# Kernel optimization log

Measured on AMD Instinct MI355X. Metric: run time of the kernel, lower is better.

Reference implementation:

```python
import jax, jax.numpy as jnp
import numpy as np

B, S, HID = 1, 2048, 2048
H, NOPE, ROPE, VDIM = 16, 128, 64, 128
QR, KVR = 1536, 512
IH, ID = 16, 128
TOPK = 512
THETA = 10000.0
EPS = 1e-6
SCALE = (NOPE + ROPE) ** -0.5
NEG = -1e9


def _cos_sin(s, dim, dtype):
    inv = 1.0 / (THETA ** (np.arange(0, dim, 2, dtype=np.float32) / dim))
    t = np.arange(s, dtype=np.float32)
    f = np.outer(t, inv)
    emb = np.concatenate([f, f], -1)
    return jnp.asarray(np.cos(emb), dtype), jnp.asarray(np.sin(emb), dtype)


def _rope(x, cos, sin):
    # x: [b,s,h,d]; cos/sin: [s,d]; NeoX-style rotate_half
    x1, x2 = jnp.split(x, 2, axis=-1)
    rot = jnp.concatenate([-x2, x1], axis=-1)
    return x * cos[None, :, None, :] + rot * sin[None, :, None, :]


def _rmsnorm(x, w):
    v = jnp.mean(x.astype(jnp.float32) ** 2, -1, keepdims=True)
    return (x.astype(jnp.float32) * jax.lax.rsqrt(v + EPS)).astype(x.dtype) * w


def _layernorm(x, w, b):
    m = jnp.mean(x, -1, keepdims=True)
    v = jnp.var(x, -1, keepdims=True)
    return (x - m) * jax.lax.rsqrt(v + EPS) * w + b


def setup_inputs() -> dict:
    key = jax.random.key(0)
    ks = jax.random.split(key, 12)
    g = lambda k, shp: jax.random.normal(k, shp, jnp.float32) * 0.02
    return {
        'hidden_states': jax.random.normal(ks[0], (B, S, HID), jnp.float32),
        'q_a_w': g(ks[1], (QR, HID)),
        'q_a_ln_w': jnp.ones((QR,), jnp.float32),
        'q_b_w': g(ks[2], (H * (NOPE + ROPE), QR)),
        'kv_a_w': g(ks[3], (KVR + ROPE, HID)),
        'kv_a_ln_w': jnp.ones((KVR,), jnp.float32),
        'kv_b_w': g(ks[4], (H * (NOPE + VDIM), KVR)),
        'o_w': g(ks[5], (HID, H * VDIM)),
        'idx_wq_b_w': g(ks[6], (IH * ID, QR)),
        'idx_wk_w': g(ks[7], (ID, HID)),
        'idx_kn_w': jnp.ones((ID,), jnp.float32),
        'idx_kn_b': jnp.zeros((ID,), jnp.float32),
        'idx_wproj_w': g(ks[8], (IH, HID)),
    }


def reference(hidden_states, q_a_w, q_a_ln_w, q_b_w, kv_a_w, kv_a_ln_w, kv_b_w, o_w,
              idx_wq_b_w, idx_wk_w, idx_kn_w, idx_kn_b, idx_wproj_w):
    b, s, _ = hidden_states.shape
    cos, sin = _cos_sin(s, ROPE, hidden_states.dtype)

    # --- MLA projections ---
    qr = _rmsnorm(hidden_states @ q_a_w.T, q_a_ln_w)                 # [b,s,QR]
    q = (qr @ q_b_w.T).reshape(b, s, H, NOPE + ROPE)
    q_nope, q_pe = q[..., :NOPE], q[..., NOPE:]
    q_pe = _rope(q_pe, cos, sin)
    ckv = hidden_states @ kv_a_w.T                                   # [b,s,KVR+ROPE]
    c_kv, k_pe = ckv[..., :KVR], ckv[..., KVR:]
    k_pe = _rope(k_pe[:, :, None, :], cos, sin)                      # [b,s,1,ROPE]
    kv = (_rmsnorm(c_kv, kv_a_ln_w) @ kv_b_w.T).reshape(b, s, H, NOPE + VDIM)
    k_nope, v = kv[..., :NOPE], kv[..., NOPE:]

    # --- DSA indexer: per-token importance scores ---
    iq = (qr @ idx_wq_b_w.T).reshape(b, s, IH, ID)
    iq = jnp.concatenate([_rope(iq[..., :ROPE], cos, sin), iq[..., ROPE:]], -1)
    ik = _layernorm(hidden_states @ idx_wk_w.T, idx_kn_w, idx_kn_b)  # [b,s,ID]
    ik_pe = _rope(ik[:, :, None, :ROPE], cos, sin)[:, :, 0, :]
    ik = jnp.concatenate([ik_pe, ik[..., ROPE:]], -1)
    iw = (hidden_states @ idx_wproj_w.T) * (IH ** -0.5)              # [b,s,IH]
    idx_scores = jnp.einsum('bqh,bhqk->bqk', iw,
                            jax.nn.relu(jnp.einsum('bqhd,bkd->bhqk', iq, ik)))
    causal = jnp.tril(jnp.ones((s, s), bool))
    idx_scores = jnp.where(causal[None], idx_scores, -jnp.inf)
    _, top_idx = jax.lax.top_k(idx_scores, TOPK)                     # [b,s,TOPK]
    bi = jnp.arange(b)[:, None, None]
    qi = jnp.arange(s)[None, :, None]
    keep = jnp.zeros((b, s, s), bool).at[bi, qi, top_idx].set(True)
    allowed = keep & causal[None]                                    # [b,s,s]

    # --- sparse top-k attention (top-k mask to -inf before softmax) ---
    qh = jnp.concatenate([q_nope, q_pe], -1)                         # [b,s,H,192]
    kh = jnp.concatenate([k_nope, jnp.broadcast_to(k_pe, (b, s, H, ROPE))], -1)
    scores = jnp.einsum('bqhd,bkhd->bhqk', qh, kh) * SCALE
    scores = jnp.where(allowed[:, None], scores, NEG)
    attn = jax.nn.softmax(scores, -1)
    out = jnp.einsum('bhqk,bkhd->bqhd', attn, v).reshape(b, s, H * VDIM)
    return out @ o_w.T
```

## Files before the change

### kernel.cpp

```cpp
#include <hip/hip_runtime.h>
#include <hip/hip_bf16.h>
#include <math.h>

#define SEQ 2048
#define HIDD 2048
#define QRANK 1536
#define KVRANK 512
#define TOPK 512
#define EPSF 1e-6f
#define SCALE_ATTN 0.07216878364870323f
#define NCAT 1680

typedef __attribute__((ext_vector_type(8))) short short8v;
typedef __attribute__((ext_vector_type(4))) short short4v;
typedef __attribute__((ext_vector_type(4))) float f32x4;

__device__ inline unsigned short f2bf(float f) {
    unsigned u = __float_as_uint(f);
    unsigned r = (u + 0x7FFFu + ((u >> 16) & 1u)) >> 16;
    return (unsigned short)r;
}
__device__ inline float bf2f(unsigned short b) {
    return __uint_as_float(((unsigned)b) << 16);
}
__device__ inline void split2(float x, unsigned short& h, unsigned short& l) {
    h = f2bf(x);
    l = f2bf(x - bf2f(h));
}

__device__ inline short4v ds_read_tr16(const void* p) {
#if __has_builtin(__builtin_amdgcn_ds_read_tr16_b64)
    return __builtin_amdgcn_ds_read_tr16_b64((short4v*)p);
#else
    const unsigned short* u = (const unsigned short*)p;
    short4v r;
    r[0] = (short)u[0]; r[1] = (short)u[16]; r[2] = (short)u[32]; r[3] = (short)u[48];
    return r;
#endif
}

__global__ void rope_table_kernel(float* __restrict__ cos_t, float* __restrict__ sin_t) {
    int s = blockIdx.x;
    int i = threadIdx.x;
    double inv = pow(10000.0, -((double)(2 * i)) / 64.0);
    double f = (double)s * inv;
    cos_t[s * 32 + i] = (float)cos(f);
    sin_t[s * 32 + i] = (float)sin(f);
}

__global__ __launch_bounds__(256) void cvt_bf16_4_kernel(
    const float* __restrict__ a, int na4, const float* __restrict__ b, int nb4,
    const float* __restrict__ c, int nc4, const float* __restrict__ d, int nd4,
    unsigned short* __restrict__ oa, unsigned short* __restrict__ ob,
    unsigned short* __restrict__ oc, unsigned short* __restrict__ od)
{
    int total = na4 + nb4 + nc4 + nd4;
    for (int i = blockIdx.x * 256 + threadIdx.x; i < total; i += gridDim.x * 256) {
        const float* src; unsigned short* dst; int j = i;
        if (j < na4) { src = a; dst = oa; }
        else if ((j -= na4) < nb4) { src = b; dst = ob; }
        else if ((j -= nb4) < nc4) { src = c; dst = oc; }
        else { j -= nc4; src = d; dst = od; }
        float4 v = ((const float4*)src)[j];
        ushort4 o;
        o.x = f2bf(v.x); o.y = f2bf(v.y); o.z = f2bf(v.z); o.w = f2bf(v.w);
        ((ushort4*)dst)[j] = o;
    }
}

__global__ __launch_bounds__(256) void wkt_kernel(const float* __restrict__ kvb,
                                                  unsigned short* __restrict__ wkt) {
    __shared__ float t[128][129];
    int h = blockIdx.x, n0 = blockIdx.y * 128;
    int tid = threadIdx.x;
    for (int it = tid; it < 128 * 32; it += 256) {
        int d = it >> 5, c4 = it & 31;
        float4 v = *(const float4*)(kvb + ((size_t)(h * 256 + d)) * 512 + n0 + c4 * 4);
        t[d][c4 * 4 + 0] = v.x; t[d][c4 * 4 + 1] = v.y;
        t[d][c4 * 4 + 2] = v.z; t[d][c4 * 4 + 3] = v.w;
    }
    __syncthreads();
    for (int it = tid; it < 128 * 32; it += 256) {
        int n = it >> 5, dc = it & 31;
        ushort4 o;
        o.x = f2bf(t[dc * 4 + 0][n]); o.y = f2bf(t[dc * 4 + 1][n]);
        o.z = f2bf(t[dc * 4 + 2][n]); o.w = f2bf(t[dc * 4 + 3][n]);
        *(ushort4*)(wkt + ((size_t)h * 512 + n0 + n) * 128 + dc * 4) = o;
    }
}

__global__ __launch_bounds__(256) void gemm_cat_split_kernel(
    const float* __restrict__ hidden, const float* __restrict__ q_a_w,
    const float* __restrict__ idx_wk_w, const float* __restrict__ idx_wproj_w,
    float* __restrict__ ccat)
{
    __shared__ __align__(16) unsigned short Ah[128 * 32], Al[128 * 32];
    __shared__ __align__(16) unsigned short Bh[128 * 32], Bl[128 * 32];
    int tid = threadIdx.x;
    int l = tid & 63, w = tid >> 6;
    int wr = w >> 1, wc = w & 1;
    int m0 = blockIdx.x * 128, n0 = blockIdx.y * 128;
    f32x4 acc[4][4] = {};
    for (int k0 = 0; k0 < HIDD; k0 += 32) {
        __syncthreads();
#pragma unroll
        for (int i = 0; i < 2; ++i) {
            int idx = tid + i * 256;
            int r = idx >> 2, cc = idx & 3;
            int sw = cc ^ (r & 3);
            {
                const float* src = hidden + (size_t)(m0 + r) * HIDD + k0 + cc * 8;
                float4 f0 = *(const float4*)src, f1 = *(const float4*)(src + 4);
                float xs[8] = {f0.x, f0.y, f0.z, f0.w, f1.x, f1.y, f1.z, f1.w};
                short8v dh, dl;
#pragma unroll
                for (int e = 0; e < 8; ++e) {
                    unsigned short hh, ll; split2(xs[e], hh, ll);
                    dh[e] = (short)hh; dl[e] = (short)ll;
                }
                *(short8v*)&Ah[r * 32 + sw * 8] = dh;
                *(short8v*)&Al[r * 32 + sw * 8] = dl;
            }
            {
                int gb = n0 + r; if (gb > NCAT - 1) gb = NCAT - 1;
                float scale = 1.f;
                const float* src;
                if (gb < 1536) src = q_a_w + (size_t)gb * HIDD;
                else if (gb < 1664) src = idx_wk_w + (size_t)(gb - 1536) * HIDD;
                else { src = idx_wproj_w + (size_t)(gb - 1664) * HIDD; scale = 0.25f; }
                src += k0 + cc * 8;
                float4 f0 = *(const float4*)src, f1 = *(const float4*)(src + 4);
                float xs[8] = {f0.x, f0.y, f0.z, f0.w, f1.x, f1.y, f1.z, f1.w};
                short8v dh, dl;
#pragma unroll
                for (int e = 0; e < 8; ++e) {
                    unsigned short hh, ll; split2(xs[e] * scale, hh, ll);
                    dh[e] = (short)hh; dl[e] = (short)ll;
                }
                *(short8v*)&Bh[r * 32 + sw * 8] = dh;
                *(short8v*)&Bl[r * 32 + sw * 8] = dl;
            }
        }
        __syncthreads();
        short8v avh[4], avl[4];
#pragma unroll
        for (int mt = 0; mt < 4; ++mt) {
            int row = wr * 64 + mt * 16 + (l & 15);
            int ch = (l >> 4) ^ (row & 3);
            avh[mt] = *(const short8v*)&Ah[row * 32 + ch * 8];
            avl[mt] = *(const short8v*)&Al[row * 32 + ch * 8];
        }
#pragma unroll
        for (int nt = 0; nt < 4; ++nt) {
            int row = wc * 64 + nt * 16 + (l & 15);
            int ch = (l >> 4) ^ (row & 3);
            short8v bvh = *(const short8v*)&Bh[row * 32 + ch * 8];
            short8v bvl = *(const short8v*)&Bl[row * 32 + ch * 8];
#pragma unroll
            for (int mt = 0; mt < 4; ++mt) {
                acc[mt][nt] = __builtin_amdgcn_mfma_f32_16x16x32_bf16(avh[mt], bvh, acc[mt][nt], 0, 0, 0);
                acc[mt][nt] = __builtin_amdgcn_mfma_f32_16x16x32_bf16(avh[mt], bvl, acc[mt][nt], 0, 0, 0);
                acc[mt][nt] = __builtin_amdgcn_mfma_f32_16x16x32_bf16(avl[mt], bvh, acc[mt][nt], 0, 0, 0);
            }
        }
    }
#pragma unroll
    for (int mt = 0; mt < 4; ++mt)
#pragma unroll
        for (int nt = 0; nt < 4; ++nt)
#pragma unroll
            for (int i = 0; i < 4; ++i) {
                int gm = m0 + wr * 64 + mt * 16 + (l >> 4) * 4 + i;
                int gn = n0 + wc * 64 + nt * 16 + (l & 15);
                if (gn < NCAT) ccat[(size_t)gm * NCAT + gn] = acc[mt][nt][i];
            }
}

__global__ __launch_bounds__(256) void gemm_iq_split_kernel(
    const float* __restrict__ qr, const float* __restrict__ wq,
    const float* __restrict__ cos_t, const float* __restrict__ sin_t,
    unsigned short* __restrict__ iqh, unsigned short* __restrict__ iql)
{
    __shared__ __align__(16) unsigned short Ah[128 * 32], Al[128 * 32];
    __shared__ __align__(16) unsigned short Bh[128 * 32], Bl[128 * 32];
    int tid = threadIdx.x;
    int l = tid & 63, w = tid >> 6;
    int wr = w >> 1, wc = w & 1;
    int m0 = blockIdx.x * 128, n0 = blockIdx.y * 128;
    int hh_ = blockIdx.y;
    f32x4 acc[4][4] = {};
    for (int k0 = 0; k0 < QRANK; k0 += 32) {
        __syncthreads();
#pragma unroll
        for (int i = 0; i < 2; ++i) {
            int idx = tid + i * 256;
            int r = idx >> 2, cc = idx & 3;
            int sw = cc ^ (r & 3);
            {
                const float* src = qr + (size_t)(m0 + r) * QRANK + k0 + cc * 8;
                float4 f0 = *(const float4*)src, f1 = *(const float4*)(src + 4);
                float xs[8] = {f0.x, f0.y, f0.z, f0.w, f1.x, f1.y, f1.z, f1.w};
                short8v dh, dl;
#pragma unroll
                for (int e = 0; e < 8; ++e) {
                    unsigned short h2, l2; split2(xs[e], h2, l2);
                    dh[e] = (short)h2; dl[e] = (short)l2;
                }
                *(short8v*)&Ah[r * 32 + sw * 8] = dh;
                *(short8v*)&Al[r * 32 + sw * 8] = dl;
            }
            {
                const float* src = wq + (size_t)(n0 + r) * QRANK + k0 + cc * 8;
                float4 f0 = *(const float4*)src, f1 = *(const float4*)(src + 4);
                float xs[8] = {f0.x, f0.y, f0.z, f0.w, f1.x, f1.y, f1.z, f1.w};
                short8v dh, dl;
#pragma unroll
                for (int e = 0; e < 8; ++e) {
                    unsigned short h2, l2; split2(xs[e], h2, l2);
                    dh[e] = (short)h2; dl[e] = (short)l2;
                }
                *(short8v*)&Bh[r * 32 + sw * 8] = dh;
                *(short8v*)&Bl[r * 32 + sw * 8] = dl;
            }
        }
        __syncthreads();
        short8v avh[4], avl[4];
#pragma unroll
        for (int mt = 0; mt < 4; ++mt) {
            int row = wr * 64 + mt * 16 + (l & 15);
            int ch = (l >> 4) ^ (row & 3);
            avh[mt] = *(const short8v*)&Ah[row * 32 + ch * 8];
            avl[mt] = *(const short8v*)&Al[row * 32 + ch * 8];
        }
#pragma unroll
        for (int nt = 0; nt < 4; ++nt) {
            int row = wc * 64 + nt * 16 + (l & 15);
            int ch = (l >> 4) ^ (row & 3);
            short8v bvh = *(const short8v*)&Bh[row * 32 + ch * 8];
            short8v bvl = *(const short8v*)&Bl[row * 32 + ch * 8];
#pragma unroll
            for (int mt = 0; mt < 4; ++mt) {
                acc[mt][nt] = __builtin_amdgcn_mfma_f32_16x16x32_bf16(avh[mt], bvh, acc[mt][nt], 0, 0, 0);
                acc[mt][nt] = __builtin_amdgcn_mfma_f32_16x16x32_bf16(avh[mt], bvl, acc[mt][nt], 0, 0, 0);
                acc[mt][nt] = __builtin_amdgcn_mfma_f32_16x16x32_bf16(avl[mt], bvh, acc[mt][nt], 0, 0, 0);
            }
        }
    }
    if (wc == 0) {
#pragma unroll
        for (int mt = 0; mt < 4; ++mt)
#pragma unroll
            for (int nt = 0; nt < 2; ++nt)
#pragma unroll
                for (int i = 0; i < 4; ++i) {
                    int q = m0 + wr * 64 + mt * 16 + (l >> 4) * 4 + i;
                    int dd = nt * 16 + (l & 15);
                    float c = cos_t[q * 32 + dd], s = sin_t[q * 32 + dd];
                    float x1 = acc[mt][nt][i], x2 = acc[mt][nt + 2][i];
                    acc[mt][nt][i] = x1 * c - x2 * s;
                    acc[mt][nt + 2][i] = x2 * c + x1 * s;
                }
    }
#pragma unroll
    for (int mt = 0; mt < 4; ++mt)
#pragma unroll
        for (int nt = 0; nt < 4; ++nt)
#pragma unroll
            for (int i = 0; i < 4; ++i) {
                int q = m0 + wr * 64 + mt * 16 + (l >> 4) * 4 + i;
                int d = wc * 64 + nt * 16 + (l & 15);
                size_t idx = ((size_t)q * 16 + hh_) * 128 + d;
                unsigned short h2, l2; split2(acc[mt][nt][i], h2, l2);
                iqh[idx] = h2; iql[idx] = l2;
            }
}

template <typename TA, typename TC>
__global__ __launch_bounds__(256) void mfma_nt_kernel(
    const TA* __restrict__ A, const unsigned short* __restrict__ B, TC* __restrict__ C,
    int M, int N, int K, int lda, int ldb, int ldc, long ab, long bb, long cb,
    const float* __restrict__ cos_t, const float* __restrict__ sin_t, int rope_mode)
{
    __shared__ __align__(16) unsigned short Asl[128 * 32];
    __shared__ __align__(16) unsigned short Bsl[128 * 32];
    int z = blockIdx.z;
    const TA* Az = A + (size_t)z * ab;
    const unsigned short* Bz = B + (size_t)z * bb;
    TC* Cz = C + (size_t)z * cb;
    int tid = threadIdx.x;
    int l = tid & 63, w = tid >> 6;
    int wr = w >> 1, wc = w & 1;
    int m0 = blockIdx.x * 128, n0 = blockIdx.y * 128;
    f32x4 acc[4][4] = {};

    for (int k0 = 0; k0 < K; k0 += 32) {
        __syncthreads();
#pragma unroll
        for (int i = 0; i < 2; ++i) {
            int idx = tid + i * 256;
            int r = idx >> 2, cc = idx & 3;
            int sw = cc ^ (r & 3);
            {
                short8v d;
                const TA* src = Az + (size_t)(m0 + r) * lda + k0 + cc * 8;
                if constexpr (sizeof(TA) == 2) {
                    d = *(const short8v*)src;
                } else {
                    float4 f0 = *(const float4*)src;
                    float4 f1 = *(const float4*)(src + 4);
                    d[0] = (short)f2bf(f0.x); d[1] = (short)f2bf(f0.y);
                    d[2] = (short)f2bf(f0.z); d[3] = (short)f2bf(f0.w);
                    d[4] = (short)f2bf(f1.x); d[5] = (short)f2bf(f1.y);
                    d[6] = (short)f2bf(f1.z); d[7] = (short)f2bf(f1.w);
                }
                *(short8v*)&Asl[r * 32 + sw * 8] = d;
            }
            {
                int gb = n0 + r; if (gb > N - 1) gb = N - 1;
                short8v d = *(const short8v*)(Bz + (size_t)gb * ldb + k0 + cc * 8);
                *(short8v*)&Bsl[r * 32 + sw * 8] = d;
            }
        }
        __syncthreads();
        short8v av[4], bv[4];
#pragma unroll
        for (int mt = 0; mt < 4; ++mt) {
            int row = wr * 64 + mt * 16 + (l & 15);
            int ch = (l >> 4) ^ (row & 3);
            av[mt] = *(const short8v*)&Asl[row * 32 + ch * 8];
        }
#pragma unroll
        for (int nt = 0; nt < 4; ++nt) {
            int row = wc * 64 + nt * 16 + (l & 15);
            int ch = (l >> 4) ^ (row & 3);
            bv[nt] = *(const short8v*)&Bsl[row * 32 + ch * 8];
        }
#pragma unroll
        for (int mt = 0; mt < 4; ++mt)
#pragma unroll
            for (int nt = 0; nt < 4; ++nt)
                acc[mt][nt] = __builtin_amdgcn_mfma_f32_16x16x32_bf16(av[mt], bv[nt], acc[mt][nt], 0, 0, 0);
    }
    if (rope_mode) {
        int gcol64 = (n0 >> 6) + wc;
        bool dorope = (rope_mode == 1) ? ((gcol64 % 3) == 2) : (gcol64 == 8);
        if (dorope) {
#pragma unroll
            for (int mt = 0; mt < 4; ++mt)
#pragma unroll
                for (int nt = 0; nt < 2; ++nt)
#pragma unroll
                    for (int i = 0; i < 4; ++i) {
                        int q = m0 + wr * 64 + mt * 16 + (l >> 4) * 4 + i;
                        int dd = nt * 16 + (l & 15);
                        float c = cos_t[q * 32 + dd], sn = sin_t[q * 32 + dd];
                        float x1 = acc[mt][nt][i], x2 = acc[mt][nt + 2][i];
                        acc[mt][nt][i] = x1 * c - x2 * sn;
                        acc[mt][nt + 2][i] = x2 * c + x1 * sn;
                    }
        }
    }
#pragma unroll
    for (int mt = 0; mt < 4; ++mt) {
#pragma unroll
        for (int nt = 0; nt < 4; ++nt) {
#pragma unroll
            for (int i = 0; i < 4; ++i) {
                int gm = m0 + wr * 64 + mt * 16 + (l >> 4) * 4 + i;
                int gn = n0 + wc * 64 + nt * 16 + (l & 15);
                if (gn < N) {
                    float v = acc[mt][nt][i];
                    if constexpr (sizeof(TC) == 4) Cz[(size_t)gm * ldc + gn] = v;
                    else Cz[(size_t)gm * ldc + gn] = f2bf(v);
                }
            }
        }
    }
}

__global__ __launch_bounds__(256) void rmsnorm_kernel(
    const float* __restrict__ in, const float* __restrict__ w, float* __restrict__ out,
    unsigned short* __restrict__ bf_out, int n, int in_stride)
{
    int row = blockIdx.x, tid = threadIdx.x;
    const float* x = in + (size_t)row * in_stride;
    float4 v[2];
    int cnt = 0;
    float ss = 0.f;
    int nf4 = n >> 2;
    for (int i = tid; i < nf4; i += 256) {
        float4 t = *(const float4*)(x + i * 4);
        v[cnt++] = t;
        ss += t.x * t.x + t.y * t.y + t.z * t.z + t.w * t.w;
    }
#pragma unroll
    for (int m = 32; m; m >>= 1) ss += __shfl_xor(ss, m);
    __shared__ float red[8];
    int wid = tid >> 6;
    if ((tid & 63) == 0) red[wid] = ss;
    __syncthreads();
    if (tid == 0) {
        float s = red[0] + red[1] + red[2] + red[3];
        red[4] = rsqrtf(s / (float)n + EPSF);
    }
    __syncthreads();
    float scale = red[4];
    cnt = 0;
    for (int i = tid; i < nf4; i += 256) {
        float4 t = v[cnt++];
        float4 wv = *(const float4*)(w + i * 4);
        float4 o;
        o.x = t.x * scale * wv.x; o.y = t.y * scale * wv.y;
        o.z = t.z * scale * wv.z; o.w = t.w * scale * wv.w;
        *(float4*)(out + (size_t)row * n + i * 4) = o;
        if (bf_out) {
            ushort4 ob;
            ob.x = f2bf(o.x); ob.y = f2bf(o.y); ob.z = f2bf(o.z); ob.w = f2bf(o.w);
            *(ushort4*)(bf_out + (size_t)row * n + i * 4) = ob;
        }
    }
}

__global__ __launch_bounds__(256) void rmsnorm_khg_kernel(
    const float* __restrict__ ckv, const float* __restrict__ w,
    unsigned short* __restrict__ khg)
{
    int row = blockIdx.x, tid = threadIdx.x;
    const float* x = ckv + (size_t)row * 576;
    float4 v = make_float4(0.f, 0.f, 0.f, 0.f);
    float ss = 0.f;
    if (tid < 128) {
        v = *(const float4*)(x + tid * 4);
        ss = v.x * v.x + v.y * v.y + v.z * v.z + v.w * v.w;
    }
#pragma unroll
    for (int mm = 32; mm; mm >>= 1) ss += __shfl_xor(ss, mm);
    __shared__ float red[8];
    if ((tid & 63) == 0) red[tid >> 6] = ss;
    __syncthreads();
    if (tid == 0) red[4] = rsqrtf((red[0] + red[1] + red[2] + red[3]) * (1.f / 512.f) + EPSF);
    __syncthreads();
    float scale = red[4];
    if (tid < 128) {
        float4 wv = *(const float4*)(w + tid * 4);
        ushort4 ob;
        ob.x = f2bf(v.x * scale * wv.x); ob.y = f2bf(v.y * scale * wv.y);
        ob.z = f2bf(v.z * scale * wv.z); ob.w = f2bf(v.w * scale * wv.w);
        *(ushort4*)(khg + (size_t)row * 576 + tid * 4) = ob;
    } else if (tid < 192) {
        khg[(size_t)row * 576 + 512 + (tid - 128)] = f2bf(x[512 + tid - 128]);
    }
}

__global__ __launch_bounds__(64) void ln_rope_split_kernel(
    const float* __restrict__ in, int stride,
    const float* __restrict__ w, const float* __restrict__ b,
    const float* __restrict__ cos_t, const float* __restrict__ sin_t,
    unsigned short* __restrict__ ikh, unsigned short* __restrict__ ikl)
{
    int row = blockIdx.x, tid = threadIdx.x;
    const float* x = in + (size_t)row * stride;
    float x0 = x[tid], x1 = x[tid + 64];
    float s = x0 + x1, ss = x0 * x0 + x1 * x1;
#pragma unroll
    for (int m = 32; m; m >>= 1) { s += __shfl_xor(s, m); ss += __shfl_xor(ss, m); }
    float mean = s * (1.f / 128.f);
    float var = ss * (1.f / 128.f) - mean * mean;
    float r = rsqrtf(var + EPSF);
    float n0 = (x0 - mean) * r * w[tid] + b[tid];
    float n1 = (x1 - mean) * r * w[tid + 64] + b[tid + 64];
    float c = cos_t[row * 32 + (tid & 31)], sn = sin_t[row * 32 + (tid & 31)];
    float other = __shfl_xor(n0, 32);
    float r0 = (tid < 32) ? (n0 * c - other * sn) : (n0 * c + other * sn);
    unsigned short h2, l2;
    split2(r0, h2, l2);
    ikh[(size_t)row * 128 + tid] = h2; ikl[(size_t)row * 128 + tid] = l2;
    split2(n1, h2, l2);
    ikh[(size_t)row * 128 + 64 + tid] = h2; ikl[(size_t)row * 128 + 64 + tid] = l2;
}

__global__ __launch_bounds__(256) void idx_scores_mfma_kernel(
    const unsigned short* __restrict__ iqh, const unsigned short* __restrict__ iql,
    const unsigned short* __restrict__ ikh, const unsigned short* __restrict__ ikl,
    const float* __restrict__ iwsrc, int iw_stride,
    float* __restrict__ scores)
{
    int q0 = blockIdx.x * 64, k0 = blockIdx.y * 64;
    int tid = threadIdx.x;
    if (k0 > q0 + 63) {
        for (int t = tid; t < 64 * 64; t += 256) {
            int r = t >> 6, c = t & 63;
            scores[(size_t)(q0 + r) * SEQ + k0 + c] = -INFINITY;
        }
        return;
    }
    __shared__ __align__(16) unsigned short skh[64 * 128], skl[64 * 128];
    __shared__ __align__(16) unsigned short sqh[64 * 128], sql[64 * 128];
    __shared__ float iws[64][16];
    int l = tid & 63, w = tid >> 6;
    for (int it = tid; it < 64 * 16; it += 256) {
        int r = it >> 4, c = it & 15;
        int sw = c ^ (r & 15);
        *(short8v*)&skh[r * 128 + sw * 8] = *(const short8v*)(ikh + (size_t)(k0 + r) * 128 + c * 8);
        *(short8v*)&skl[r * 128 + sw * 8] = *(const short8v*)(ikl + (size_t)(k0 + r) * 128 + c * 8);
    }
    {
        int r = tid >> 2, c = tid & 3;
        *(float4*)&iws[r][c * 4] = *(const float4*)(iwsrc + (size_t)(q0 + r) * iw_stride + c * 4);
    }
    __syncthreads();
    short8v bhr[4][4], blr[4][4];
#pragma unroll
    for (int nt = 0; nt < 4; ++nt)
#pragma unroll
        for (int ks = 0; ks < 4; ++ks) {
            int brow = nt * 16 + (l & 15);
            int bch = ((l >> 4) + ks * 4) ^ (brow & 15);
            bhr[nt][ks] = *(const short8v*)&skh[brow * 128 + bch * 8];
            blr[nt][ks] = *(const short8v*)&skl[brow * 128 + bch * 8];
        }
    f32x4 acc[4] = {};
    for (int h = 0; h < 16; ++h) {
        __syncthreads();
        for (int it = tid; it < 64 * 16; it += 256) {
            int r = it >> 4, c = it & 15;
            int sw = c ^ (r & 15);
            size_t base = ((size_t)(q0 + r) * 16 + h) * 128 + c * 8;
            *(short8v*)&sqh[r * 128 + sw * 8] = *(const short8v*)(iqh + base);
            *(short8v*)&sql[r * 128 + sw * 8] = *(const short8v*)(iql + base);
        }
        __syncthreads();
        f32x4 dot[4] = {};
#pragma unroll
        for (int ks = 0; ks < 4; ++ks) {
            int arow = w * 16 + (l & 15);
            int ach = ((l >> 4) + ks * 4) ^ (arow & 15);
            short8v ah = *(const short8v*)&sqh[arow * 128 + ach * 8];
            short8v al = *(const short8v*)&sql[arow * 128 + ach * 8];
#pragma unroll
            for (int nt = 0; nt < 4; ++nt) {
                dot[nt] = __builtin_amdgcn_mfma_f32_16x16x32_bf16(ah, bhr[nt][ks], dot[nt], 0, 0, 0);
                dot[nt] = __builtin_amdgcn_mfma_f32_16x16x32_bf16(ah, blr[nt][ks], dot[nt], 0, 0, 0);
                dot[nt] = __builtin_amdgcn_mfma_f32_16x16x32_bf16(al, bhr[nt][ks], dot[nt], 0, 0, 0);
            }
        }
#pragma unroll
        for (int nt = 0; nt < 4; ++nt)
#pragma unroll
            for (int i = 0; i < 4; ++i) {
                float wv = iws[w * 16 + (l >> 4) * 4 + i][h];
                acc[nt][i] += wv * fmaxf(dot[nt][i], 0.f);
            }
    }
#pragma unroll
    for (int nt = 0; nt < 4; ++nt)
#pragma unroll
        for (int i = 0; i < 4; ++i) {
            int q = q0 + w * 16 + (l >> 4) * 4 + i;
            int k = k0 + nt * 16 + (l & 15);
            scores[(size_t)q * SEQ + k] = (k <= q) ? acc[nt][i] : -INFINITY;
        }
}

__global__ __launch_bounds__(1024) void topk_kernel(
    const float* __restrict__ scores, int* __restrict__ sel)
{
    int qi = blockIdx.x, tid = threadIdx.x;
    __shared__ unsigned long long keys[2048];
    const float* srow = scores + (size_t)qi * SEQ;
#pragma unroll
    for (int r = 0; r < 2; ++r) {
        int k = tid + r * 1024;
        unsigned u = __float_as_uint(srow[k]);
        unsigned mv = (u & 0x80000000u) ? ~u : (u | 0x80000000u);
        keys[k] = ((unsigned long long)mv << 32) | (unsigned)(2047 - k);
    }
    for (int ksz = 2; ksz <= 2048; ksz <<= 1) {
        for (int j = ksz >> 1; j > 0; j >>= 1) {
            __syncthreads();
#pragma unroll 1
            for (int r = 0; r < 2; ++r) {
                int i = tid + r * 1024;
                int ixj = i ^ j;
                if (ixj > i) {
                    unsigned long long a = keys[i], b = keys[ixj];
                    bool dir = ((i & ksz) == 0);
                    if ((a < b) == dir) { keys[i] = b; keys[ixj] = a; }
                }
            }
        }
    }
    __syncthreads();
    if (tid < TOPK) {
        int k = 2047 - (int)(keys[tid] & 0xFFFFFFFFu);
        sel[(size_t)qi * TOPK + tid] = (tid <= qi) ? k : -1;
    }
}

__global__ __launch_bounds__(256) void attn_mfma_kernel(
    const unsigned short* __restrict__ qabs,
    const float* __restrict__ qsrc,
    const unsigned short* __restrict__ khg,
    const int* __restrict__ sel,
    unsigned short* __restrict__ ocomp)
{
    __shared__ __align__(16) char smem[77568];
    unsigned short* plds = (unsigned short*)(smem + 74752);
    float* smax = (float*)(smem + 76800);
    float* ssum = (float*)(smem + 77056);
    int* selb   = (int*)(smem + 77312);

    const int qi = blockIdx.x;
    const int tid = threadIdx.x;
    const int l = tid & 63, w = tid >> 6;
    const int lg = l >> 4, lr = l & 15;
    const int nv = min(TOPK, qi + 1);
    const int ntile = (nv + 63) >> 6;
    const int krow = w * 16 + lr;

    short8v aq[18];
    {
        const unsigned short* qa = qabs + ((size_t)qi * 16 + lr) * 512 + lg * 8;
#pragma unroll
        for (int ks = 0; ks < 16; ++ks)
            aq[ks] = *(const short8v*)(qa + ks * 32);
        const float* qp = qsrc + (size_t)qi * 3072 + lr * 192 + 128 + lg * 8;
#pragma unroll
        for (int ks = 0; ks < 2; ++ks) {
            float4 f0 = *(const float4*)(qp + ks * 32);
            float4 f1 = *(const float4*)(qp + ks * 32 + 4);
            short8v d;
            d[0] = (short)f2bf(f0.x); d[1] = (short)f2bf(f0.y);
            d[2] = (short)f2bf(f0.z); d[3] = (short)f2bf(f0.w);
            d[4] = (short)f2bf(f1.x); d[5] = (short)f2bf(f1.y);
            d[6] = (short)f2bf(f1.z); d[7] = (short)f2bf(f1.w);
            aq[16 + ks] = d;
        }
    }

    const int sbase = krow * 32 + (lg >> 1) * 2080 + (lg & 1) * 16;
    const int vboff = w * 16640 + lg * 256 + lr * 2;

    float m[4] = {-1e30f, -1e30f, -1e30f, -1e30f};
    float lsum[4] = {0.f, 0.f, 0.f, 0.f};
    f32x4 oacc[8] = {};

    for (int t = 0; t < ntile; ++t) {
        const int j0 = t * 64;
        __syncthreads();
        if (tid < 64) {
            int sv = sel[(size_t)qi * TOPK + j0 + tid];
            selb[tid] = sv < 0 ? 0 : sv;
        }
        __syncthreads();
        for (int it = tid; it < 64 * 64; it += 256) {
            int key = it >> 6, c = it & 63;
            short8v v = *(const short8v*)(khg + (size_t)selb[key] * 576 + c * 8);
            *(short8v*)(smem + (c >> 1) * 2080 + key * 32 + (c & 1) * 16) = v;
        }
        for (int it = tid; it < 64 * 8; it += 256) {
            int key = it >> 3, c = it & 7;
            short8v v = *(const short8v*)(khg + (size_t)selb[key] * 576 + 512 + c * 8);
            *(short8v*)(smem + 66560 + ((key * 128 + c * 16) ^ ((key & 7) << 4))) = v;
        }
        __syncthreads();
        f32x4 s = {};
#pragma unroll
        for (int ks = 0; ks < 16; ++ks) {
            short8v b = *(const short8v*)(smem + sbase + ks * 4160);
            s = __builtin_amdgcn_mfma_f32_16x16x32_bf16(aq[ks], b, s, 0, 0, 0);
        }
#pragma unroll
        for (int ks = 0; ks < 2; ++ks) {
            short8v b = *(const short8v*)(smem + 66560 +
                ((krow * 128 + ks * 64 + lg * 16) ^ ((krow & 7) << 4)));
            s = __builtin_amdgcn_mfma_f32_16x16x32_bf16(aq[16 + ks], b, s, 0, 0, 0);
        }
        bool kvalid = (j0 + krow) < nv;
#pragma unroll
        for (int i = 0; i < 4; ++i)
            s[i] = kvalid ? s[i] * SCALE_ATTN : -1e30f;
        float tm[4];
#pragma unroll
        for (int i = 0; i < 4; ++i) tm[i] = s[i];
#pragma unroll
        for (int sh = 1; sh < 16; sh <<= 1)
#pragma unroll
            for (int i = 0; i < 4; ++i) tm[i] = fmaxf(tm[i], __shfl_xor(tm[i], sh));
        if (lr == 0) *(float4*)&smax[w * 16 + lg * 4] = make_float4(tm[0], tm[1], tm[2], tm[3]);
        __syncthreads();
        float mn[4], scl[4];
#pragma unroll
        for (int i = 0; i < 4; ++i) {
            int h = lg * 4 + i;
            float tmax = fmaxf(fmaxf(smax[h], smax[16 + h]), fmaxf(smax[32 + h], smax[48 + h]));
            mn[i] = fmaxf(m[i], tmax);
            scl[i] = __expf(m[i] - mn[i]);
            m[i] = mn[i];
        }
        float p[4], rs[4];
#pragma unroll
        for (int i = 0; i < 4; ++i) { p[i] = __expf(s[i] - mn[i]); rs[i] = p[i]; }
#pragma unroll
        for (int sh = 1; sh < 16; sh <<= 1)
#pragma unroll
            for (int i = 0; i < 4; ++i) rs[i] += __shfl_xor(rs[i], sh);
        if (lr == 0) *(float4*)&ssum[w * 16 + lg * 4] = make_float4(rs[0], rs[1], rs[2], rs[3]);
        {
            ushort4 pb;
            pb.x = f2bf(p[0]); pb.y = f2bf(p[1]); pb.z = f2bf(p[2]); pb.w = f2bf(p[3]);
            *(ushort4*)&plds[(w * 16 + lr) * 16 + lg * 4] = pb;
        }
        __syncthreads();
#pragma unroll
        for (int i = 0; i < 4; ++i) {
            int h = lg * 4 + i;
            float ts = ssum[h] + ssum[16 + h] + ssum[32 + h] + ssum[48 + h];
            lsum[i] = lsum[i] * scl[i] + ts;
        }
#pragma unroll
        for (int nt = 0; nt < 8; ++nt)
#pragma unroll
            for (int i = 0; i < 4; ++i) oacc[nt][i] *= scl[i];
#pragma unroll
        for (int kb = 0; kb < 2; ++kb) {
            short8v af;
#pragma unroll
            for (int j = 0; j < 8; ++j)
                af[j] = (short)plds[(kb * 32 + lg * 8 + j) * 16 + lr];
#pragma unroll
            for (int nt = 0; nt < 8; ++nt) {
                const char* a = smem + vboff + kb * 1024 + nt * 2080;
                short4v t0 = ds_read_tr16(a);
                short4v t1 = ds_read_tr16(a + 128);
                short8v bf = __builtin_shufflevector(t0, t1, 0, 1, 2, 3, 4, 5, 6, 7);
                oacc[nt] = __builtin_amdgcn_mfma_f32_16x16x32_bf16(af, bf, oacc[nt], 0, 0, 0);
            }
        }
    }
    float inv[4];
#pragma unroll
    for (int i = 0; i < 4; ++i) inv[i] = 1.f / lsum[i];
    unsigned short* ob = ocomp + (size_t)qi * 16 * 512;
#pragma unroll
    for (int nt = 0; nt < 8; ++nt) {
        int d = w * 128 + nt * 16 + lr;
#pragma unroll
        for (int i = 0; i < 4; ++i) {
            int h = lg * 4 + i;
            ob[h * 512 + d] = f2bf(oacc[nt][i] * inv[i]);
        }
    }
}

extern "C" void kernel_launch(void* const* d_in, const int* in_sizes, int n_in,
                              void* d_out, int out_size, void* d_ws, size_t ws_size,
                              hipStream_t stream) {
    (void)in_sizes; (void)n_in; (void)out_size; (void)ws_size;
    const float* hidden      = (const float*)d_in[0];
    const float* q_a_w       = (const float*)d_in[1];
    const float* q_a_ln_w    = (const float*)d_in[2];
    const float* q_b_w       = (const float*)d_in[3];
    const float* kv_a_w      = (const float*)d_in[4];
    const float* kv_a_ln_w   = (const float*)d_in[5];
    const float* kv_b_w      = (const float*)d_in[6];
    const float* o_w         = (const float*)d_in[7];
    const float* idx_wq_b_w  = (const float*)d_in[8];
    const float* idx_wk_w    = (const float*)d_in[9];
    const float* idx_kn_w    = (const float*)d_in[10];
    const float* idx_kn_b    = (const float*)d_in[11];
    const float* idx_wproj_w = (const float*)d_in[12];
    float* out = (float*)d_out;

    char* ws = (char*)d_ws;
    size_t off = 0;
    auto alloc = [&](size_t nbytes) -> void* {
        void* p = ws + off;
        off = (off + nbytes + 255) & ~(size_t)255;
        return p;
    };
    float* cos_t = (float*)alloc((size_t)SEQ * 32 * 4);
    float* sin_t = (float*)alloc((size_t)SEQ * 32 * 4);
    float* qbuf  = (float*)alloc((size_t)SEQ * 3072 * 4);
    float* ckv   = (float*)alloc((size_t)SEQ * 576 * 4);
    int*   sel   = (int*)alloc((size_t)SEQ * TOPK * 4);
    unsigned short* khg      = (unsigned short*)alloc((size_t)SEQ * 576 * 2);
    unsigned short* attno_bf = (unsigned short*)alloc((size_t)SEQ * 2048 * 2);
    unsigned short* qr_bf    = (unsigned short*)alloc((size_t)SEQ * QRANK * 2);
    unsigned short* q_b_bf   = (unsigned short*)alloc((size_t)3072 * QRANK * 2);
    unsigned short* kv_a_bf  = (unsigned short*)alloc((size_t)576 * HIDD * 2);
    unsigned short* o_w_bf   = (unsigned short*)alloc((size_t)HIDD * 2048 * 2);
    unsigned short* kv_b_bf  = (unsigned short*)alloc((size_t)4096 * 512 * 2);
    unsigned short* wkt      = (unsigned short*)alloc((size_t)16 * 512 * 128 * 2);
    size_t mark = off;
    float* qr    = (float*)alloc((size_t)SEQ * QRANK * 4);
    float* ccat  = (float*)alloc((size_t)SEQ * NCAT * 4);
    float* scores = (float*)alloc((size_t)SEQ * SEQ * 4);
    unsigned short* iqh = (unsigned short*)alloc((size_t)SEQ * 2048 * 2);
    unsigned short* iql = (unsigned short*)alloc((size_t)SEQ * 2048 * 2);
    unsigned short* ikh = (unsigned short*)alloc((size_t)SEQ * 128 * 2);
    unsigned short* ikl = (unsigned short*)alloc((size_t)SEQ * 128 * 2);
    off = mark;
    unsigned short* qabsb = (unsigned short*)alloc((size_t)SEQ * 16 * 512 * 2);
    unsigned short* ocomp = (unsigned short*)alloc((size_t)SEQ * 16 * 512 * 2);

    rope_table_kernel<<<dim3(SEQ), dim3(32), 0, stream>>>(cos_t, sin_t);

    cvt_bf16_4_kernel<<<2048, 256, 0, stream>>>(
        q_b_w, 3072 * QRANK / 4, kv_a_w, 576 * HIDD / 4,
        o_w, HIDD * 2048 / 4, kv_b_w, 4096 * 512 / 4,
        q_b_bf, kv_a_bf, o_w_bf, kv_b_bf);
    wkt_kernel<<<dim3(16, 4), 256, 0, stream>>>(kv_b_w, wkt);

    gemm_cat_split_kernel<<<dim3(16, 14), 256, 0, stream>>>(hidden, q_a_w, idx_wk_w, idx_wproj_w, ccat);

    rmsnorm_kernel<<<SEQ, 256, 0, stream>>>(ccat, q_a_ln_w, qr, qr_bf, QRANK, NCAT);

    ln_rope_split_kernel<<<SEQ, 64, 0, stream>>>(ccat + 1536, NCAT, idx_kn_w, idx_kn_b, cos_t, sin_t, ikh, ikl);

    mfma_nt_kernel<unsigned short, float><<<dim3(16, 24, 1), 256, 0, stream>>>(
        qr_bf, q_b_bf, qbuf, SEQ, 3072, QRANK, QRANK, QRANK, 3072, 0L, 0L, 0L,
        cos_t, sin_t, 1);

    mfma_nt_kernel<float, float><<<dim3(16, 5, 1), 256, 0, stream>>>(
        hidden, kv_a_bf, ckv, SEQ, 576, HIDD, HIDD, HIDD, 576, 0L, 0L, 0L,
        cos_t, sin_t, 2);
    rmsnorm_khg_kernel<<<SEQ, 256, 0, stream>>>(ckv, kv_a_ln_w, khg);

    gemm_iq_split_kernel<<<dim3(16, 16), 256, 0, stream>>>(qr, idx_wq_b_w, cos_t, sin_t, iqh, iql);

    idx_scores_mfma_kernel<<<dim3(32, 32), 256, 0, stream>>>(iqh, iql, ikh, ikl, ccat + 1664, NCAT, scores);
    topk_kernel<<<SEQ, 1024, 0, stream>>>(scores, sel);

    mfma_nt_kernel<float, unsigned short><<<dim3(16, 4, 16), 256, 0, stream>>>(
        qbuf, wkt, qabsb, SEQ, 512, 128, 3072, 128, 16 * 512,
        192L, 512L * 128L, 512L, nullptr, nullptr, 0);

    attn_mfma_kernel<<<SEQ, 256, 0, stream>>>(qabsb, qbuf, khg, sel, ocomp);

    mfma_nt_kernel<unsigned short, unsigned short><<<dim3(16, 1, 16), 256, 0, stream>>>(
        ocomp, kv_b_bf + (size_t)128 * 512, attno_bf, SEQ, 128, 512,
        16 * 512, 512, 2048, 512L, 256L * 512L, 128L, nullptr, nullptr, 0);

    mfma_nt_kernel<unsigned short, float><<<dim3(16, 16, 1), 256, 0, stream>>>(
        attno_bf, o_w_bf, out, SEQ, HIDD, 2048, 2048, 2048, HIDD, 0L, 0L, 0L,
        nullptr, nullptr, 0);
}
```

Measured before the change: 882.8 us.

## Pre-split fp32 operands to bf16 hi/lo and prefetch attention gathers into registers

Adds a conversion kernel that splits hidden states and the concatenated projection weights into bf16 high/low halves once, instead of inside every GEMM tile load. It also has rmsnorm emit the low half of qr so the indexer GEMM can load bf16 pairs directly. Separately, the sparse attention kernel now prefetches the next tile's gathered K/V rows into registers while the current tile computes, which removes one barrier and the shared-memory index buffer. The cost is extra workspace, an added pass over the weights each call, and higher register pressure in the attention kernel.

```diff
diff --git a/kernel.cpp b/kernel.cpp
--- a/kernel.cpp
+++ b/kernel.cpp
@@ -68,6 +68,48 @@
     }
 }
 
+__global__ __launch_bounds__(256) void cvt_split3_kernel(
+    const float* __restrict__ hidden, const float* __restrict__ q_a_w,
+    const float* __restrict__ idx_wk_w, const float* __restrict__ idx_wproj_w,
+    const float* __restrict__ wq,
+    unsigned short* __restrict__ hidh, unsigned short* __restrict__ hidl,
+    unsigned short* __restrict__ catwh, unsigned short* __restrict__ catwl,
+    unsigned short* __restrict__ wqh, unsigned short* __restrict__ wql)
+{
+    const int nhid4 = HIDD * HIDD / 4;
+    const int ncat4 = NCAT * HIDD / 4;
+    const int nwq4  = HIDD * QRANK / 4;
+    int total = nhid4 + ncat4 + nwq4;
+    for (int i = blockIdx.x * 256 + threadIdx.x; i < total; i += gridDim.x * 256) {
+        int j = i;
+        const float4* s4;
+        unsigned short *dh, *dl;
+        float scale = 1.f;
+        if (j < nhid4) {
+            s4 = (const float4*)hidden + j; dh = hidh; dl = hidl;
+        } else if ((j -= nhid4) < ncat4) {
+            int row = (j * 4) >> 11;
+            dh = catwh; dl = catwl;
+            if (row < 1536) s4 = (const float4*)q_a_w + j;
+            else if (row < 1664) s4 = (const float4*)idx_wk_w + (j - 1536 * 512);
+            else { s4 = (const float4*)idx_wproj_w + (j - 1664 * 512); scale = 0.25f; }
+        } else {
+            j -= ncat4;
+            s4 = (const float4*)wq + j; dh = wqh; dl = wql;
+        }
+        float4 v = *s4;
+        float xs[4] = {v.x * scale, v.y * scale, v.z * scale, v.w * scale};
+        ushort4 oh, ol;
+        unsigned short h2, l2;
+        split2(xs[0], h2, l2); oh.x = h2; ol.x = l2;
+        split2(xs[1], h2, l2); oh.y = h2; ol.y = l2;
+        split2(xs[2], h2, l2); oh.z = h2; ol.z = l2;
+        split2(xs[3], h2, l2); oh.w = h2; ol.w = l2;
+        ((ushort4*)dh)[j] = oh;
+        ((ushort4*)dl)[j] = ol;
+    }
+}
+
 __global__ __launch_bounds__(256) void wkt_kernel(const float* __restrict__ kvb,
                                                   unsigned short* __restrict__ wkt) {
     __shared__ float t[128][129];
@@ -92,6 +134,8 @@
 __global__ __launch_bounds__(256) void gemm_cat_split_kernel(
     const float* __restrict__ hidden, const float* __restrict__ q_a_w,
     const float* __restrict__ idx_wk_w, const float* __restrict__ idx_wproj_w,
+    const unsigned short* __restrict__ hidh, const unsigned short* __restrict__ hidl,
+    const unsigned short* __restrict__ catwh, const unsigned short* __restrict__ catwl,
     float* __restrict__ ccat)
 {
     __shared__ __align__(16) unsigned short Ah[128 * 32], Al[128 * 32];
@@ -100,6 +144,7 @@
     int l = tid & 63, w = tid >> 6;
     int wr = w >> 1, wc = w & 1;
     int m0 = blockIdx.x * 128, n0 = blockIdx.y * 128;
+    const bool pre = (hidh != nullptr);
     f32x4 acc[4][4] = {};
     for (int k0 = 0; k0 < HIDD; k0 += 32) {
         __syncthreads();
@@ -108,37 +153,46 @@
             int idx = tid + i * 256;
             int r = idx >> 2, cc = idx & 3;
             int sw = cc ^ (r & 3);
-            {
-                const float* src = hidden + (size_t)(m0 + r) * HIDD + k0 + cc * 8;
-                float4 f0 = *(const float4*)src, f1 = *(const float4*)(src + 4);
-                float xs[8] = {f0.x, f0.y, f0.z, f0.w, f1.x, f1.y, f1.z, f1.w};
-                short8v dh, dl;
-#pragma unroll
-                for (int e = 0; e < 8; ++e) {
-                    unsigned short hh, ll; split2(xs[e], hh, ll);
-                    dh[e] = (short)hh; dl[e] = (short)ll;
+            int gb = n0 + r; if (gb > NCAT - 1) gb = NCAT - 1;
+            if (pre) {
+                size_t abase = (size_t)(m0 + r) * HIDD + k0 + cc * 8;
+                *(short8v*)&Ah[r * 32 + sw * 8] = *(const short8v*)(hidh + abase);
+                *(short8v*)&Al[r * 32 + sw * 8] = *(const short8v*)(hidl + abase);
+                size_t bbase = (size_t)gb * HIDD + k0 + cc * 8;
+                *(short8v*)&Bh[r * 32 + sw * 8] = *(const short8v*)(catwh + bbase);
+                *(short8v*)&Bl[r * 32 + sw * 8] = *(const short8v*)(catwl + bbase);
+            } else {
+                {
+                    const float* src = hidden + (size_t)(m0 + r) * HIDD + k0 + cc * 8;
+                    float4 f0 = *(const float4*)src, f1 = *(const float4*)(src + 4);
+                    float xs[8] = {f0.x, f0.y, f0.z, f0.w, f1.x, f1.y, f1.z, f1.w};
+                    short8v dh, dl;
+#pragma unroll
+                    for (int e = 0; e < 8; ++e) {
+                        unsigned short hh, ll; split2(xs[e], hh, ll);
+                        dh[e] = (short)hh; dl[e] = (short)ll;
+                    }
+                    *(short8v*)&Ah[r * 32 + sw * 8] = dh;
+                    *(short8v*)&Al[r * 32 + sw * 8] = dl;
                 }
-                *(short8v*)&Ah[r * 32 + sw * 8] = dh;
-                *(short8v*)&Al[r * 32 + sw * 8] = dl;
-            }
-            {
-                int gb = n0 + r; if (gb > NCAT - 1) gb = NCAT - 1;
-                float scale = 1.f;
-                const float* src;
-                if (gb < 1536) src = q_a_w + (size_t)gb * HIDD;
-                else if (gb < 1664) src = idx_wk_w + (size_t)(gb - 1536) * HIDD;
-                else { src = idx_wproj_w + (size_t)(gb - 1664) * HIDD; scale = 0.25f; }
-                src += k0 + cc * 8;
-                float4 f0 = *(const float4*)src, f1 = *(const float4*)(src + 4);
-                float xs[8] = {f0.x, f0.y, f0.z, f0.w, f1.x, f1.y, f1.z, f1.w};
-                short8v dh, dl;
-#pragma unroll
-                for (int e = 0; e < 8; ++e) {
-                    unsigned short hh, ll; split2(xs[e] * scale, hh, ll);
-                    dh[e] = (short)hh; dl[e] = (short)ll;
+                {
+                    float scale = 1.f;
+                    const float* src;
+                    if (gb < 1536) src = q_a_w + (size_t)gb * HIDD;
+                    else if (gb < 1664) src = idx_wk_w + (size_t)(gb - 1536) * HIDD;
+                    else { src = idx_wproj_w + (size_t)(gb - 1664) * HIDD; scale = 0.25f; }
+                    src += k0 + cc * 8;
+                    float4 f0 = *(const float4*)src, f1 = *(const float4*)(src + 4);
+                    float xs[8] = {f0.x, f0.y, f0.z, f0.w, f1.x, f1.y, f1.z, f1.w};
+                    short8v dh, dl;
+#pragma unroll
+                    for (int e = 0; e < 8; ++e) {
+                        unsigned short hh, ll; split2(xs[e] * scale, hh, ll);
+                        dh[e] = (short)hh; dl[e] = (short)ll;
+                    }
+                    *(short8v*)&Bh[r * 32 + sw * 8] = dh;
+                    *(short8v*)&Bl[r * 32 + sw * 8] = dl;
                 }
-                *(short8v*)&Bh[r * 32 + sw * 8] = dh;
-                *(short8v*)&Bl[r * 32 + sw * 8] = dl;
             }
         }
         __syncthreads();
@@ -178,6 +232,8 @@
 
 __global__ __launch_bounds__(256) void gemm_iq_split_kernel(
     const float* __restrict__ qr, const float* __restrict__ wq,
+    const unsigned short* __restrict__ qrh, const unsigned short* __restrict__ qrl,
+    const unsigned short* __restrict__ wqh, const unsigned short* __restrict__ wql,
     const float* __restrict__ cos_t, const float* __restrict__ sin_t,
     unsigned short* __restrict__ iqh, unsigned short* __restrict__ iql)
 {
@@ -188,6 +244,7 @@
     int wr = w >> 1, wc = w & 1;
     int m0 = blockIdx.x * 128, n0 = blockIdx.y * 128;
     int hh_ = blockIdx.y;
+    const bool pre = (wqh != nullptr);
     f32x4 acc[4][4] = {};
     for (int k0 = 0; k0 < QRANK; k0 += 32) {
         __syncthreads();
@@ -196,31 +253,40 @@
             int idx = tid + i * 256;
             int r = idx >> 2, cc = idx & 3;
             int sw = cc ^ (r & 3);
-            {
-                const float* src = qr + (size_t)(m0 + r) * QRANK + k0 + cc * 8;
-                float4 f0 = *(const float4*)src, f1 = *(const float4*)(src + 4);
-                float xs[8] = {f0.x, f0.y, f0.z, f0.w, f1.x, f1.y, f1.z, f1.w};
-                short8v dh, dl;
-#pragma unroll
-                for (int e = 0; e < 8; ++e) {
-                    unsigned short h2, l2; split2(xs[e], h2, l2);
-                    dh[e] = (short)h2; dl[e] = (short)l2;
+            if (pre) {
+                size_t abase = (size_t)(m0 + r) * QRANK + k0 + cc * 8;
+                *(short8v*)&Ah[r * 32 + sw * 8] = *(const short8v*)(qrh + abase);
+                *(short8v*)&Al[r * 32 + sw * 8] = *(const short8v*)(qrl + abase);
+                size_t bbase = (size_t)(n0 + r) * QRANK + k0 + cc * 8;
+                *(short8v*)&Bh[r * 32 + sw * 8] = *(const short8v*)(wqh + bbase);
+                *(short8v*)&Bl[r * 32 + sw * 8] = *(const short8v*)(wql + bbase);
+            } else {
+                {
+                    const float* src = qr + (size_t)(m0 + r) * QRANK + k0 + cc * 8;
+                    float4 f0 = *(const float4*)src, f1 = *(const float4*)(src + 4);
+                    float xs[8] = {f0.x, f0.y, f0.z, f0.w, f1.x, f1.y, f1.z, f1.w};
+                    short8v dh, dl;
+#pragma unroll
+                    for (int e = 0; e < 8; ++e) {
+                        unsigned short h2, l2; split2(xs[e], h2, l2);
+                        dh[e] = (short)h2; dl[e] = (short)l2;
+                    }
+                    *(short8v*)&Ah[r * 32 + sw * 8] = dh;
+                    *(short8v*)&Al[r * 32 + sw * 8] = dl;
                 }
-                *(short8v*)&Ah[r * 32 + sw * 8] = dh;
-                *(short8v*)&Al[r * 32 + sw * 8] = dl;
-            }
-            {
-                const float* src = wq + (size_t)(n0 + r) * QRANK + k0 + cc * 8;
-                float4 f0 = *(const float4*)src, f1 = *(const float4*)(src + 4);
-                float xs[8] = {f0.x, f0.y, f0.z, f0.w, f1.x, f1.y, f1.z, f1.w};
-                short8v dh, dl;
-#pragma unroll
-                for (int e = 0; e < 8; ++e) {
-                    unsigned short h2, l2; split2(xs[e], h2, l2);
-                    dh[e] = (short)h2; dl[e] = (short)l2;
+                {
+                    const float* src = wq + (size_t)(n0 + r) * QRANK + k0 + cc * 8;
+                    float4 f0 = *(const float4*)src, f1 = *(const float4*)(src + 4);
+                    float xs[8] = {f0.x, f0.y, f0.z, f0.w, f1.x, f1.y, f1.z, f1.w};
+                    short8v dh, dl;
+#pragma unroll
+                    for (int e = 0; e < 8; ++e) {
+                        unsigned short h2, l2; split2(xs[e], h2, l2);
+                        dh[e] = (short)h2; dl[e] = (short)l2;
+                    }
+                    *(short8v*)&Bh[r * 32 + sw * 8] = dh;
+                    *(short8v*)&Bl[r * 32 + sw * 8] = dl;
                 }
-                *(short8v*)&Bh[r * 32 + sw * 8] = dh;
-                *(short8v*)&Bl[r * 32 + sw * 8] = dl;
             }
         }
         __syncthreads();
@@ -380,7 +446,8 @@
 
 __global__ __launch_bounds__(256) void rmsnorm_kernel(
     const float* __restrict__ in, const float* __restrict__ w, float* __restrict__ out,
-    unsigned short* __restrict__ bf_out, int n, int in_stride)
+    unsigned short* __restrict__ bf_out, unsigned short* __restrict__ bf_lo,
+    int n, int in_stride)
 {
     int row = blockIdx.x, tid = threadIdx.x;
     const float* x = in + (size_t)row * in_stride;
@@ -417,6 +484,12 @@
             ushort4 ob;
             ob.x = f2bf(o.x); ob.y = f2bf(o.y); ob.z = f2bf(o.z); ob.w = f2bf(o.w);
             *(ushort4*)(bf_out + (size_t)row * n + i * 4) = ob;
+            if (bf_lo) {
+                ushort4 ol;
+                ol.x = f2bf(o.x - bf2f(ob.x)); ol.y = f2bf(o.y - bf2f(ob.y));
+                ol.z = f2bf(o.z - bf2f(ob.z)); ol.w = f2bf(o.w - bf2f(ob.w));
+                *(ushort4*)(bf_lo + (size_t)row * n + i * 4) = ol;
+            }
         }
     }
 }
@@ -604,11 +677,10 @@
     const int* __restrict__ sel,
     unsigned short* __restrict__ ocomp)
 {
-    __shared__ __align__(16) char smem[77568];
+    __shared__ __align__(16) char smem[77312];
     unsigned short* plds = (unsigned short*)(smem + 74752);
     float* smax = (float*)(smem + 76800);
     float* ssum = (float*)(smem + 77056);
-    int* selb   = (int*)(smem + 77312);
 
     const int qi = blockIdx.x;
     const int tid = threadIdx.x;
@@ -617,6 +689,10 @@
     const int nv = min(TOPK, qi + 1);
     const int ntile = (nv + 63) >> 6;
     const int krow = w * 16 + lr;
+
+    const int ck = tid >> 6, cc = tid & 63;
+    const int pk = tid >> 3, pc = tid & 7;
+    const int* selrow = sel + (size_t)qi * TOPK;
 
     short8v aq[18];
     {
@@ -638,6 +714,20 @@
         }
     }
 
+    short8v vreg[16], preg[2];
+#pragma unroll
+    for (int j = 0; j < 16; ++j) {
+        int sv = selrow[ck + 4 * j];
+        if (sv < 0) sv = 0;
+        vreg[j] = *(const short8v*)(khg + (size_t)sv * 576 + cc * 8);
+    }
+#pragma unroll
+    for (int j = 0; j < 2; ++j) {
+        int sv = selrow[pk + 32 * j];
+        if (sv < 0) sv = 0;
+        preg[j] = *(const short8v*)(khg + (size_t)sv * 576 + 512 + pc * 8);
+    }
+
     const int sbase = krow * 32 + (lg >> 1) * 2080 + (lg & 1) * 16;
     const int vboff = w * 16640 + lg * 256 + lr * 2;
 
@@ -648,22 +738,32 @@
     for (int t = 0; t < ntile; ++t) {
         const int j0 = t * 64;
         __syncthreads();
-        if (tid < 64) {
-            int sv = sel[(size_t)qi * TOPK + j0 + tid];
-            selb[tid] = sv < 0 ? 0 : sv;
-        }
-        __syncthreads();
-        for (int it = tid; it < 64 * 64; it += 256) {
-            int key = it >> 6, c = it & 63;
-            short8v v = *(const short8v*)(khg + (size_t)selb[key] * 576 + c * 8);
-            *(short8v*)(smem + (c >> 1) * 2080 + key * 32 + (c & 1) * 16) = v;
-        }
-        for (int it = tid; it < 64 * 8; it += 256) {
-            int key = it >> 3, c = it & 7;
-            short8v v = *(const short8v*)(khg + (size_t)selb[key] * 576 + 512 + c * 8);
-            *(short8v*)(smem + 66560 + ((key * 128 + c * 16) ^ ((key & 7) << 4))) = v;
-        }
-        __syncthreads();
+#pragma unroll
+        for (int j = 0; j < 16; ++j) {
+            int key = ck + 4 * j;
+            *(short8v*)(smem + (cc >> 1) * 2080 + key * 32 + (cc & 1) * 16) = vreg[j];
+        }
+#pragma unroll
+        for (int j = 0; j < 2; ++j) {
+            int key = pk + 32 * j;
+            *(short8v*)(smem + 66560 + ((key * 128 + pc * 16) ^ ((key & 7) << 4))) = preg[j];
+        }
+        __syncthreads();
+        if (t + 1 < ntile) {
+            int j1 = j0 + 64;
+#pragma unroll
+            for (int j = 0; j < 16; ++j) {
+                int sv = selrow[j1 + ck + 4 * j];
+                if (sv < 0) sv = 0;
+                vreg[j] = *(const short8v*)(khg + (size_t)sv * 576 + cc * 8);
+            }
+#pragma unroll
+            for (int j = 0; j < 2; ++j) {
+                int sv = selrow[j1 + pk + 32 * j];
+                if (sv < 0) sv = 0;
+                preg[j] = *(const short8v*)(khg + (size_t)sv * 576 + 512 + pc * 8);
+            }
+        }
         f32x4 s = {};
 #pragma unroll
         for (int ks = 0; ks < 16; ++ks) {
@@ -756,7 +856,7 @@
 extern "C" void kernel_launch(void* const* d_in, const int* in_sizes, int n_in,
                               void* d_out, int out_size, void* d_ws, size_t ws_size,
                               hipStream_t stream) {
-    (void)in_sizes; (void)n_in; (void)out_size; (void)ws_size;
+    (void)in_sizes; (void)n_in; (void)out_size;
     const float* hidden      = (const float*)d_in[0];
     const float* q_a_w       = (const float*)d_in[1];
     const float* q_a_ln_w    = (const float*)d_in[2];
@@ -800,6 +900,17 @@
     unsigned short* iql = (unsigned short*)alloc((size_t)SEQ * 2048 * 2);
     unsigned short* ikh = (unsigned short*)alloc((size_t)SEQ * 128 * 2);
     unsigned short* ikl = (unsigned short*)alloc((size_t)SEQ * 128 * 2);
+    unsigned short* hidh  = (unsigned short*)alloc((size_t)HIDD * HIDD * 2);
+    unsigned short* hidl  = (unsigned short*)alloc((size_t)HIDD * HIDD * 2);
+    unsigned short* catwh = (unsigned short*)alloc((size_t)NCAT * HIDD * 2);
+    unsigned short* catwl = (unsigned short*)alloc((size_t)NCAT * HIDD * 2);
+    unsigned short* wqh   = (unsigned short*)alloc((size_t)HIDD * QRANK * 2);
+    unsigned short* wql   = (unsigned short*)alloc((size_t)HIDD * QRANK * 2);
+    unsigned short* qr_l  = (unsigned short*)alloc((size_t)SEQ * QRANK * 2);
+    bool fast = (off <= ws_size);
+    if (!fast) {
+        hidh = hidl = catwh = catwl = wqh = wql = qr_l = nullptr;
+    }
     off = mark;
     unsigned short* qabsb = (unsigned short*)alloc((size_t)SEQ * 16 * 512 * 2);
     unsigned short* ocomp = (unsigned short*)alloc((size_t)SEQ * 16 * 512 * 2);
@@ -811,10 +922,15 @@
         o_w, HIDD * 2048 / 4, kv_b_w, 4096 * 512 / 4,
         q_b_bf, kv_a_bf, o_w_bf, kv_b_bf);
     wkt_kernel<<<dim3(16, 4), 256, 0, stream>>>(kv_b_w, wkt);
-
-    gemm_cat_split_kernel<<<dim3(16, 14), 256, 0, stream>>>(hidden, q_a_w, idx_wk_w, idx_wproj_w, ccat);
-
-    rmsnorm_kernel<<<SEQ, 256, 0, stream>>>(ccat, q_a_ln_w, qr, qr_bf, QRANK, NCAT);
+    if (fast)
+        cvt_split3_kernel<<<2048, 256, 0, stream>>>(
+            hidden, q_a_w, idx_wk_w, idx_wproj_w, idx_wq_b_w,
+            hidh, hidl, catwh, catwl, wqh, wql);
+
+    gemm_cat_split_kernel<<<dim3(16, 14), 256, 0, stream>>>(
+        hidden, q_a_w, idx_wk_w, idx_wproj_w, hidh, hidl, catwh, catwl, ccat);
+
+    rmsnorm_kernel<<<SEQ, 256, 0, stream>>>(ccat, q_a_ln_w, qr, qr_bf, qr_l, QRANK, NCAT);
 
     ln_rope_split_kernel<<<SEQ, 64, 0, stream>>>(ccat + 1536, NCAT, idx_kn_w, idx_kn_b, cos_t, sin_t, ikh, ikl);
 
@@ -827,7 +943,8 @@
         cos_t, sin_t, 2);
     rmsnorm_khg_kernel<<<SEQ, 256, 0, stream>>>(ckv, kv_a_ln_w, khg);
 
-    gemm_iq_split_kernel<<<dim3(16, 16), 256, 0, stream>>>(qr, idx_wq_b_w, cos_t, sin_t, iqh, iql);
+    gemm_iq_split_kernel<<<dim3(16, 16), 256, 0, stream>>>(
+        qr, idx_wq_b_w, qr_bf, qr_l, wqh, wql, cos_t, sin_t, iqh, iql);
 
     idx_scores_mfma_kernel<<<dim3(32, 32), 256, 0, stream>>>(iqh, iql, ikh, ikl, ccat + 1664, NCAT, scores);
     topk_kernel<<<SEQ, 1024, 0, stream>>>(scores, sel);
```

Result: no change. 883.9 us (+0.1%).
